# Kernel tuning notes

Measured on AMD Instinct MI355X. Metric: run time of the kernel, lower is better.

## Reference

```python
import jax, jax.numpy as jnp
import numpy as np

# static config matching init_kwargs / setup
T = 0.1      # temperature
MARG = 0.0   # margin m
NEG_IOU = 0.5
K = 1        # pos_topk
WEIGHT = 1.0
P = 2080     # number of True entries in mask2d (triu of 64x64)


def _normalize(x, axis=-1, eps=1e-12):
    n = jnp.sqrt(jnp.sum(x * x, axis=axis, keepdims=True))
    return x / jnp.maximum(n, eps)


def _log_ce(pos_scores, all_scores, neg_mask, t, m):
    # pos_scores: (..., K); all_scores: (..., K or 1, L); neg_mask broadcastable to all_scores
    pos_logit = (pos_scores - m) / t
    pos_exp = jnp.exp(pos_logit)
    neg_exp_sum = jnp.sum(jnp.exp(all_scores / t) * neg_mask.astype(all_scores.dtype), axis=-1)
    loss = -(pos_logit - jnp.log(pos_exp + neg_exp_sum))
    return jnp.mean(loss)


def setup_inputs() -> dict:
    key = jax.random.key(0)
    k1, k2, k3, k4 = jax.random.split(key, 4)
    S, C, N, B, M = 64, 256, 64, 16, 128
    video_feats = jax.random.normal(k1, (S, C, N, N), dtype=jnp.float32)
    sents_feats = jax.random.normal(k2, (S, C), dtype=jnp.float32)
    iou2d = jax.random.uniform(k3, (S, N, N), dtype=jnp.float32)
    iou2ds = jax.random.uniform(k4, (M, N, N), dtype=jnp.float32)
    num_sentences = jnp.full((B,), 4, dtype=jnp.int32)   # sum == S
    num_targets = jnp.full((S,), 2, dtype=jnp.int32)     # sum == M
    mask2d = jnp.triu(jnp.ones((N, N), dtype=bool))      # P = 2080 valid proposals
    return {
        "video_feats": video_feats, "sents_feats": sents_feats,
        "iou2d": iou2d, "iou2ds": iou2ds,
        "num_sentences": num_sentences, "num_targets": num_targets,
        "mask2d": mask2d,
    }


def reference(video_feats, sents_feats, iou2d, iou2ds, num_sentences, num_targets, mask2d):
    S, C, N, _ = video_feats.shape
    B = num_sentences.shape[0]
    M = iou2ds.shape[0]

    # flat proposal indices (static count P)
    mask_idx = jnp.nonzero(mask2d.reshape(-1), size=P)[0]

    # scatter maps
    scatter_b2s = jnp.concatenate([jnp.zeros((1,), jnp.int32),
                                   jnp.cumsum(num_sentences)[:-1].astype(jnp.int32)])  # (B,)
    scatter_m2s = jnp.repeat(jnp.arange(S), num_targets, total_repeat_length=M)        # (M,)
    scatter_s2b = jnp.repeat(jnp.arange(B), num_sentences, total_repeat_length=S)      # (S,)

    # select valid proposals: (S,C,P) -> (S,P,C)
    vf = video_feats.reshape(S, C, N * N)[:, :, mask_idx].transpose(0, 2, 1)
    iou2d_f = iou2d.reshape(S, N * N)[:, mask_idx]    # (S,P)
    iou2ds_f = iou2ds.reshape(M, N * N)[:, mask_idx]  # (M,P)

    vf = _normalize(vf, axis=-1)          # (S,P,C)
    sf = _normalize(sents_feats, axis=-1) # (S,C)

    # top-K proposals per moment
    topk_idxs = jax.lax.top_k(iou2ds_f, K)[1]                         # (M,K)
    allm_vf = vf[scatter_m2s]                                         # (M,P,C)
    topk_vf = jnp.take_along_axis(allm_vf, topk_idxs[:, :, None], 1)  # (M,K,C)

    # inter-video loss
    inter_video_pos = jnp.sum(topk_vf * sf[scatter_m2s][:, None, :], axis=-1)  # (M,K)
    inter_video_all = jnp.einsum('mkc,sc->mks', topk_vf, sf)                   # (M,K,S)
    eye_mask = ~jnp.eye(S, dtype=bool)
    inter_video_neg_mask = eye_mask[scatter_m2s][:, None, :]                   # (M,1,S)
    loss_inter_video = _log_ce(inter_video_pos, inter_video_all, inter_video_neg_mask, T, MARG)

    # inter-query loss
    inter_query_pos = inter_video_pos                                  # (M,K)
    vf_b = vf[scatter_b2s].reshape(B * P, C)                           # one sentence-rep per video
    inter_query_all = jnp.einsum('sc,qc->sq', sf, vf_b)[:, None, :]    # (S,1,B*P)

    # pos_mask: row s has its video block b=scatter_s2b[s] set to (iou2d > neg_iou)
    s2v_pos = iou2d_f > NEG_IOU                                        # (S,P)
    pos_mask = jnp.zeros((S, B, P), dtype=bool)
    pos_mask = pos_mask.at[jnp.arange(S), scatter_s2b].set(s2v_pos)
    pos_mask = pos_mask.reshape(S, B * P)
    inter_query_neg_mask = (~pos_mask)[:, None, :]                     # (S,1,B*P)

    loss_inter_query = _log_ce(inter_query_pos,
                               inter_query_all[scatter_m2s],
                               inter_query_neg_mask[scatter_m2s], T, MARG)

    return (loss_inter_video + loss_inter_query) * WEIGHT
```

## Files before the change

### kernel.cpp

```cpp
#include <hip/hip_runtime.h>
#include <math.h>

#define C 256
#define NN 4096
#define SDIM 64
#define T_INV 10.0f
#define NEG_IOU_TH 0.5f
#define SG 32
#define QTILE 256
#define QTILES (NN / QTILE)

__device__ __forceinline__ float wave_reduce_sum(float v) {
    #pragma unroll
    for (int off = 32; off > 0; off >>= 1) v += __shfl_xor(v, off, 64);
    return v;
}

__global__ void k_prep(const float* __restrict__ sents,
                       const int* __restrict__ num_sentences,
                       const int* __restrict__ num_targets,
                       int B, int S, int M,
                       float* __restrict__ sfT, int* __restrict__ b2s,
                       int* __restrict__ s2b, int* __restrict__ m2s,
                       float* __restrict__ denomq, int* __restrict__ counter) {
    __shared__ float red[4];
    int s = blockIdx.x, tid = threadIdx.x;
    float v = sents[(size_t)s * C + tid];
    float ssq = wave_reduce_sum(v * v);
    int lane = tid & 63, wave = tid >> 6;
    if (lane == 0) red[wave] = ssq;
    __syncthreads();
    float tot = red[0] + red[1] + red[2] + red[3];
    sfT[(size_t)tid * S + s] = v * (1.0f / fmaxf(sqrtf(tot), 1e-12f));

    if (blockIdx.x == 0) {
        if (tid < S) denomq[tid] = 0.f;
        if (tid == 0) {
            *counter = 0;
            int acc = 0;
            for (int b = 0; b < B; ++b) {
                b2s[b] = acc;
                int nsb = num_sentences[b];
                for (int k = 0; k < nsb; ++k) s2b[acc + k] = b;
                acc += nsb;
            }
            int mi = 0;
            for (int si = 0; si < S; ++si) {
                int nt = num_targets[si];
                for (int k = 0; k < nt; ++k) m2s[mi++] = si;
            }
        }
    }
}

__global__ void __launch_bounds__(256)
k_main(const float* __restrict__ vf, const float* __restrict__ iou2d,
       const float* __restrict__ iou2ds, const int* __restrict__ num_sentences,
       const float* __restrict__ sfT, const int* __restrict__ b2s,
       const int* __restrict__ m2s,
       float* __restrict__ pos, float* __restrict__ negiv,
       float* __restrict__ denomq, int* __restrict__ counter,
       float* __restrict__ out, int S, int B, int M, int nq, int ntot) {
    __shared__ float red[4];
    __shared__ int   sidx[4];
    __shared__ float dw[4][SDIM];
    __shared__ int   bestflat;
    __shared__ int   amlast;
    __shared__ float tv[C];
    __shared__ float sc4[256];

    int bid = blockIdx.x, tid = threadIdx.x;
    int lane = tid & 63, wave = tid >> 6;

    if (bid >= M) {
        int qb   = bid - M;
        int tile = qb & (QTILES - 1);
        int rem  = qb >> 4;
        int b    = rem & 15;
        int g    = rem >> 4;
        int sb = b2s[b];
        int ns = num_sentences[b];

        int flat = tile * QTILE + tid;
        const float* vp = vf + (size_t)sb * C * NN + flat;
        const float4* sq = (const float4*)sfT + (size_t)g * 8;

        float acc[SG];
        #pragma unroll
        for (int s = 0; s < SG; ++s) acc[s] = 0.f;
        float ssq = 0.f;

        #pragma unroll 4
        for (int c = 0; c < C; ++c) {
            float v = vp[(size_t)c * NN];
            ssq += v * v;
            const float4* sqc = sq + (size_t)c * (SDIM / 4);
            #pragma unroll
            for (int k = 0; k < SG / 4; ++k) {
                float4 q4 = sqc[k];
                acc[k * 4 + 0] += q4.x * v;
                acc[k * 4 + 1] += q4.y * v;
                acc[k * 4 + 2] += q4.z * v;
                acc[k * 4 + 3] += q4.w * v;
            }
        }

        int r = flat >> 6, cc = flat & 63;
        bool valid = (cc >= r);
        float scale = (1.0f / fmaxf(sqrtf(ssq), 1e-12f)) * T_INV;

        unsigned long long excl = 0ull;
        for (int i = 0; i < ns; ++i)
            if (iou2d[(size_t)(sb + i) * NN + flat] > NEG_IOU_TH)
                excl |= (1ull << (sb + i));
        if (!valid) excl = ~0ull;

        unsigned mask32 = (unsigned)(excl >> (g * 32));
        #pragma unroll
        for (int i = 0; i < SG; ++i)
            acc[i] = ((mask32 >> i) & 1u) ? 0.f : expf(acc[i] * scale);

        #pragma unroll
        for (int off = 16; off >= 1; off >>= 1) {
            int bsel = lane & off;
            #pragma unroll
            for (int i = 0; i < off; ++i) {
                float keep = bsel ? acc[off + i] : acc[i];
                float send = bsel ? acc[i] : acc[off + i];
                acc[i] = keep + __shfl_xor(send, off, 64);
            }
        }
        float tot_s = acc[0] + __shfl_xor(acc[0], 32, 64);
        if (lane < 32) dw[wave][lane] = tot_s;
        __syncthreads();
        if (tid < 32)
            atomicAdd(&denomq[g * 32 + tid],
                      dw[0][tid] + dw[1][tid] + dw[2][tid] + dw[3][tid]);
    } else {
        int m = bid;
        int s_m = m2s[m];

        float bv = -1e30f; int bi = NN;
        #pragma unroll
        for (int j = 0; j < NN / 256; ++j) {
            int flat = tid + j * 256;
            int rr = flat >> 6, cc = flat & 63;
            if (cc >= rr) {
                float val = iou2ds[(size_t)m * NN + flat];
                if (val > bv || (val == bv && flat < bi)) { bv = val; bi = flat; }
            }
        }
        #pragma unroll
        for (int off = 32; off > 0; off >>= 1) {
            float ov = __shfl_xor(bv, off, 64);
            int   oi = __shfl_xor(bi, off, 64);
            if (ov > bv || (ov == bv && oi < bi)) { bv = ov; bi = oi; }
        }
        if (lane == 0) { red[wave] = bv; sidx[wave] = bi; }
        __syncthreads();
        if (tid == 0) {
            float v0 = red[0]; int i0 = sidx[0];
            for (int w = 1; w < 4; ++w)
                if (red[w] > v0 || (red[w] == v0 && sidx[w] < i0)) { v0 = red[w]; i0 = sidx[w]; }
            bestflat = i0;
        }
        __syncthreads();
        int flat = bestflat;

        float v = vf[((size_t)s_m * C + tid) * NN + flat];
        float ssq = wave_reduce_sum(v * v);
        if (lane == 0) red[wave] = ssq;
        __syncthreads();
        float tot = red[0] + red[1] + red[2] + red[3];
        tv[tid] = v * (1.0f / fmaxf(sqrtf(tot), 1e-12f));
        __syncthreads();

        {
            int s = tid & 63, cg = tid >> 6;
            float d = 0.f;
            for (int j = 0; j < 64; ++j) {
                int c2 = cg * 64 + j;
                d += tv[c2] * sfT[(size_t)c2 * S + s];
            }
            sc4[cg * 64 + s] = d;
        }
        __syncthreads();
        if (tid < 64) {
            float d = sc4[tid] + sc4[64 + tid] + sc4[128 + tid] + sc4[192 + tid];
            if (tid == s_m) atomicExch(&pos[m], d);
            float e = (tid == s_m) ? 0.f : expf(d * T_INV);
            e = wave_reduce_sum(e);
            if (tid == 0) atomicExch(&negiv[m], e);
        }
    }

    __syncthreads();
    if (tid == 0) {
        __threadfence();
        int old = atomicAdd(counter, 1);
        amlast = (old == ntot - 1) ? 1 : 0;
    }
    __syncthreads();
    if (!amlast) return;

    __threadfence();
    float val = 0.f;
    for (int m = tid; m < M; m += 256) {
        int s = m2s[m];
        float pl  = atomicAdd(&pos[m], 0.f) * T_INV;
        float niv = atomicAdd(&negiv[m], 0.f);
        float dq  = atomicAdd(&denomq[s], 0.f);
        float pe = expf(pl);
        val += -(pl - logf(pe + niv)) + -(pl - logf(pe + dq));
    }
    val = wave_reduce_sum(val);
    if (lane == 0) dw[0][wave] = val;
    __syncthreads();
    if (tid == 0) out[0] = (dw[0][0] + dw[0][1] + dw[0][2] + dw[0][3]) / (float)M;
}

extern "C" void kernel_launch(void* const* d_in, const int* in_sizes, int n_in,
                              void* d_out, int out_size, void* d_ws, size_t ws_size,
                              hipStream_t stream) {
    const float* video_feats   = (const float*)d_in[0];
    const float* sents_feats   = (const float*)d_in[1];
    const float* iou2d         = (const float*)d_in[2];
    const float* iou2ds        = (const float*)d_in[3];
    const int*   num_sentences = (const int*)d_in[4];
    const int*   num_targets   = (const int*)d_in[5];

    const int S = in_sizes[2] / NN;
    const int B = in_sizes[4];
    const int M = in_sizes[3] / NN;

    float* sfT    = (float*)d_ws;
    float* pos    = sfT + (size_t)C * 64;
    float* negiv  = pos + M;
    float* denomq = negiv + M;
    int*   b2s    = (int*)(denomq + S);
    int*   s2b    = b2s + B;
    int*   m2s    = s2b + S;
    int*   counter = m2s + M;

    const int nq   = QTILES * B * (SDIM / SG);
    const int ntot = M + nq;

    k_prep<<<S, C, 0, stream>>>(sents_feats, num_sentences, num_targets,
                                B, S, M, sfT, b2s, s2b, m2s, denomq, counter);
    k_main<<<ntot, 256, 0, stream>>>(video_feats, iou2d, iou2ds, num_sentences,
                                     sfT, b2s, m2s, pos, negiv, denomq, counter,
                                     (float*)d_out, S, B, M, nq, ntot);
}
```

Baseline: 383.7 us.

## Fuse prep into main kernel, stage sentence tile in LDS, two proposals per thread

```diff
diff --git a/kernel.cpp b/kernel.cpp
--- a/kernel.cpp
+++ b/kernel.cpp
@@ -7,8 +7,10 @@
 #define T_INV 10.0f
 #define NEG_IOU_TH 0.5f
 #define SG 32
-#define QTILE 256
-#define QTILES (NN / QTILE)
+#define FL 2
+#define QT (256 * FL)
+#define QTILES (NN / QT)
+#define PAD 36
 
 __device__ __forceinline__ float wave_reduce_sum(float v) {
     #pragma unroll
@@ -16,58 +18,19 @@
     return v;
 }
 
-__global__ void k_prep(const float* __restrict__ sents,
-                       const int* __restrict__ num_sentences,
-                       const int* __restrict__ num_targets,
-                       int B, int S, int M,
-                       float* __restrict__ sfT, int* __restrict__ b2s,
-                       int* __restrict__ s2b, int* __restrict__ m2s,
-                       float* __restrict__ denomq, int* __restrict__ counter) {
-    __shared__ float red[4];
-    int s = blockIdx.x, tid = threadIdx.x;
-    float v = sents[(size_t)s * C + tid];
-    float ssq = wave_reduce_sum(v * v);
-    int lane = tid & 63, wave = tid >> 6;
-    if (lane == 0) red[wave] = ssq;
-    __syncthreads();
-    float tot = red[0] + red[1] + red[2] + red[3];
-    sfT[(size_t)tid * S + s] = v * (1.0f / fmaxf(sqrtf(tot), 1e-12f));
-
-    if (blockIdx.x == 0) {
-        if (tid < S) denomq[tid] = 0.f;
-        if (tid == 0) {
-            *counter = 0;
-            int acc = 0;
-            for (int b = 0; b < B; ++b) {
-                b2s[b] = acc;
-                int nsb = num_sentences[b];
-                for (int k = 0; k < nsb; ++k) s2b[acc + k] = b;
-                acc += nsb;
-            }
-            int mi = 0;
-            for (int si = 0; si < S; ++si) {
-                int nt = num_targets[si];
-                for (int k = 0; k < nt; ++k) m2s[mi++] = si;
-            }
-        }
-    }
-}
-
 __global__ void __launch_bounds__(256)
-k_main(const float* __restrict__ vf, const float* __restrict__ iou2d,
-       const float* __restrict__ iou2ds, const int* __restrict__ num_sentences,
-       const float* __restrict__ sfT, const int* __restrict__ b2s,
-       const int* __restrict__ m2s,
-       float* __restrict__ pos, float* __restrict__ negiv,
+k_main(const float* __restrict__ vf, const float* __restrict__ sents,
+       const float* __restrict__ iou2d, const float* __restrict__ iou2ds,
+       const int* __restrict__ num_sentences, const int* __restrict__ num_targets,
        float* __restrict__ denomq, int* __restrict__ counter,
-       float* __restrict__ out, int S, int B, int M, int nq, int ntot) {
+       float* __restrict__ pos, float* __restrict__ negiv, int* __restrict__ msent,
+       float* __restrict__ out, int S, int B, int M, int ntot) {
+    __shared__ float smem[C * PAD + SG];
     __shared__ float red[4];
     __shared__ int   sidx[4];
-    __shared__ float dw[4][SDIM];
+    __shared__ float dw[4][SG];
     __shared__ int   bestflat;
     __shared__ int   amlast;
-    __shared__ float tv[C];
-    __shared__ float sc4[256];
 
     int bid = blockIdx.x, tid = threadIdx.x;
     int lane = tid & 63, wave = tid >> 6;
@@ -75,77 +38,122 @@
     if (bid >= M) {
         int qb   = bid - M;
         int tile = qb & (QTILES - 1);
-        int rem  = qb >> 4;
-        int b    = rem & 15;
-        int g    = rem >> 4;
-        int sb = b2s[b];
+        int b    = (qb >> 3) & 15;
+        int g    = qb >> 7;
+
+        int sb = 0;
+        for (int i = 0; i < b; ++i) sb += num_sentences[i];
         int ns = num_sentences[b];
 
-        int flat = tile * QTILE + tid;
-        const float* vp = vf + (size_t)sb * C * NN + flat;
-        const float4* sq = (const float4*)sfT + (size_t)g * 8;
-
-        float acc[SG];
-        #pragma unroll
-        for (int s = 0; s < SG; ++s) acc[s] = 0.f;
-        float ssq = 0.f;
-
-        #pragma unroll 4
+        float* sT = smem;
+        float* sn = smem + C * PAD;
+        if (tid < SG) sn[tid] = 0.f;
+        __syncthreads();
+        {
+            int s  = tid >> 3;
+            int c0 = (tid & 7) * 32;
+            const float* sp = sents + (size_t)(g * SG + s) * C + c0;
+            float ssq = 0.f;
+            #pragma unroll
+            for (int j = 0; j < 32; j += 4) {
+                float4 x = *(const float4*)(sp + j);
+                sT[(c0 + j + 0) * PAD + s] = x.x;
+                sT[(c0 + j + 1) * PAD + s] = x.y;
+                sT[(c0 + j + 2) * PAD + s] = x.z;
+                sT[(c0 + j + 3) * PAD + s] = x.w;
+                ssq += x.x*x.x + x.y*x.y + x.z*x.z + x.w*x.w;
+            }
+            atomicAdd(&sn[s], ssq);
+        }
+        __syncthreads();
+        if (tid < SG) sn[tid] = 1.0f / fmaxf(sqrtf(sn[tid]), 1e-12f);
+        __syncthreads();
+
+        int flat0 = tile * QT + tid * FL;
+        const float2* vp = (const float2*)(vf + (size_t)sb * C * NN + flat0);
+
+        float accA[SG], accB[SG];
+        #pragma unroll
+        for (int i = 0; i < SG; ++i) { accA[i] = 0.f; accB[i] = 0.f; }
+        float ssx = 0.f, ssy = 0.f;
+
+        #pragma unroll 2
         for (int c = 0; c < C; ++c) {
-            float v = vp[(size_t)c * NN];
-            ssq += v * v;
-            const float4* sqc = sq + (size_t)c * (SDIM / 4);
+            float2 v = vp[(size_t)c * (NN / 2)];
+            ssx += v.x * v.x; ssy += v.y * v.y;
+            const float4* sr = (const float4*)&sT[c * PAD];
             #pragma unroll
             for (int k = 0; k < SG / 4; ++k) {
-                float4 q4 = sqc[k];
-                acc[k * 4 + 0] += q4.x * v;
-                acc[k * 4 + 1] += q4.y * v;
-                acc[k * 4 + 2] += q4.z * v;
-                acc[k * 4 + 3] += q4.w * v;
-            }
-        }
-
-        int r = flat >> 6, cc = flat & 63;
-        bool valid = (cc >= r);
-        float scale = (1.0f / fmaxf(sqrtf(ssq), 1e-12f)) * T_INV;
-
-        unsigned long long excl = 0ull;
-        for (int i = 0; i < ns; ++i)
-            if (iou2d[(size_t)(sb + i) * NN + flat] > NEG_IOU_TH)
-                excl |= (1ull << (sb + i));
-        if (!valid) excl = ~0ull;
-
-        unsigned mask32 = (unsigned)(excl >> (g * 32));
-        #pragma unroll
-        for (int i = 0; i < SG; ++i)
-            acc[i] = ((mask32 >> i) & 1u) ? 0.f : expf(acc[i] * scale);
+                float4 q4 = sr[k];
+                accA[k*4+0] += q4.x * v.x;  accB[k*4+0] += q4.x * v.y;
+                accA[k*4+1] += q4.y * v.x;  accB[k*4+1] += q4.y * v.y;
+                accA[k*4+2] += q4.z * v.x;  accB[k*4+2] += q4.z * v.y;
+                accA[k*4+3] += q4.w * v.x;  accB[k*4+3] += q4.w * v.y;
+            }
+        }
+
+        int fA = flat0, fB = flat0 + 1;
+        bool vA = ((fA & 63) >= (fA >> 6));
+        bool vB = ((fB & 63) >= (fB >> 6));
+        float sclA = (1.0f / fmaxf(sqrtf(ssx), 1e-12f)) * T_INV;
+        float sclB = (1.0f / fmaxf(sqrtf(ssy), 1e-12f)) * T_INV;
+
+        unsigned long long bitsA = 0ull, bitsB = 0ull;
+        for (int i = 0; i < ns; ++i) {
+            const float* row = iou2d + (size_t)(sb + i) * NN;
+            if (vA && row[fA] > NEG_IOU_TH) bitsA |= (1ull << (sb + i));
+            if (vB && row[fB] > NEG_IOU_TH) bitsB |= (1ull << (sb + i));
+        }
+        unsigned mA = vA ? (unsigned)(bitsA >> (g * SG)) : 0xffffffffu;
+        unsigned mB = vB ? (unsigned)(bitsB >> (g * SG)) : 0xffffffffu;
+
+        #pragma unroll
+        for (int i = 0; i < SG; ++i) {
+            float inv = sn[i];
+            float e = 0.f;
+            if (!((mA >> i) & 1u)) e += expf(accA[i] * inv * sclA);
+            if (!((mB >> i) & 1u)) e += expf(accB[i] * inv * sclB);
+            accA[i] = e;
+        }
 
         #pragma unroll
         for (int off = 16; off >= 1; off >>= 1) {
             int bsel = lane & off;
             #pragma unroll
             for (int i = 0; i < off; ++i) {
-                float keep = bsel ? acc[off + i] : acc[i];
-                float send = bsel ? acc[i] : acc[off + i];
-                acc[i] = keep + __shfl_xor(send, off, 64);
-            }
-        }
-        float tot_s = acc[0] + __shfl_xor(acc[0], 32, 64);
+                float keep = bsel ? accA[off + i] : accA[i];
+                float send = bsel ? accA[i] : accA[off + i];
+                accA[i] = keep + __shfl_xor(send, off, 64);
+            }
+        }
+        float tot_s = accA[0] + __shfl_xor(accA[0], 32, 64);
         if (lane < 32) dw[wave][lane] = tot_s;
         __syncthreads();
-        if (tid < 32)
-            atomicAdd(&denomq[g * 32 + tid],
+        if (tid < SG)
+            atomicAdd(&denomq[g * SG + tid],
                       dw[0][tid] + dw[1][tid] + dw[2][tid] + dw[3][tid]);
     } else {
         int m = bid;
-        int s_m = m2s[m];
+        int s_m = 0;
+        {
+            int acc2 = 0;
+            for (int s2 = 0; s2 < SDIM; ++s2) {
+                int nt = num_targets[s2];
+                if (m >= acc2 && m < acc2 + nt) s_m = s2;
+                acc2 += nt;
+            }
+        }
+
+        float* tv = smem;
+        float* pd = smem + C;
+        float* ps = smem + C + 256;
 
         float bv = -1e30f; int bi = NN;
         #pragma unroll
         for (int j = 0; j < NN / 256; ++j) {
             int flat = tid + j * 256;
-            int rr = flat >> 6, cc = flat & 63;
-            if (cc >= rr) {
+            int rr = flat >> 6, cc2 = flat & 63;
+            if (cc2 >= rr) {
                 float val = iou2ds[(size_t)m * NN + flat];
                 if (val > bv || (val == bv && flat < bi)) { bv = val; bi = flat; }
             }
@@ -176,21 +184,28 @@
         __syncthreads();
 
         {
-            int s = tid & 63, cg = tid >> 6;
-            float d = 0.f;
-            for (int j = 0; j < 64; ++j) {
-                int c2 = cg * 64 + j;
-                d += tv[c2] * sfT[(size_t)c2 * S + s];
-            }
-            sc4[cg * 64 + s] = d;
-        }
-        __syncthreads();
-        if (tid < 64) {
-            float d = sc4[tid] + sc4[64 + tid] + sc4[128 + tid] + sc4[192 + tid];
-            if (tid == s_m) atomicExch(&pos[m], d);
-            float e = (tid == s_m) ? 0.f : expf(d * T_INV);
+            int s2 = tid >> 2, q = tid & 3;
+            const float4* sp = (const float4*)(sents + (size_t)s2 * C + q * 64);
+            const float4* tp = (const float4*)(tv + q * 64);
+            float d = 0.f, ss = 0.f;
+            #pragma unroll
+            for (int j = 0; j < 16; ++j) {
+                float4 x = sp[j];
+                float4 t = tp[j];
+                d  += x.x*t.x + x.y*t.y + x.z*t.z + x.w*t.w;
+                ss += x.x*x.x + x.y*x.y + x.z*x.z + x.w*x.w;
+            }
+            pd[tid] = d; ps[tid] = ss;
+        }
+        __syncthreads();
+        if (tid < SDIM) {
+            float dt = pd[tid*4+0] + pd[tid*4+1] + pd[tid*4+2] + pd[tid*4+3];
+            float st = ps[tid*4+0] + ps[tid*4+1] + ps[tid*4+2] + ps[tid*4+3];
+            float dd = dt * (1.0f / fmaxf(sqrtf(st), 1e-12f));
+            if (tid == s_m) atomicExch(&pos[m], dd);
+            float e = (tid == s_m) ? 0.f : expf(dd * T_INV);
             e = wave_reduce_sum(e);
-            if (tid == 0) atomicExch(&negiv[m], e);
+            if (tid == 0) { atomicExch(&negiv[m], e); atomicExch(&msent[m], s_m); }
         }
     }
 
@@ -205,11 +220,11 @@
 
     __threadfence();
     float val = 0.f;
-    for (int m = tid; m < M; m += 256) {
-        int s = m2s[m];
-        float pl  = atomicAdd(&pos[m], 0.f) * T_INV;
-        float niv = atomicAdd(&negiv[m], 0.f);
-        float dq  = atomicAdd(&denomq[s], 0.f);
+    for (int m2 = tid; m2 < M; m2 += 256) {
+        int   sm2 = atomicAdd(&msent[m2], 0);
+        float pl  = atomicAdd(&pos[m2], 0.f) * T_INV;
+        float niv = atomicAdd(&negiv[m2], 0.f);
+        float dq  = atomicAdd(&denomq[sm2], 0.f);
         float pe = expf(pl);
         val += -(pl - logf(pe + niv)) + -(pl - logf(pe + dq));
     }
@@ -233,21 +248,19 @@
     const int B = in_sizes[4];
     const int M = in_sizes[3] / NN;
 
-    float* sfT    = (float*)d_ws;
-    float* pos    = sfT + (size_t)C * 64;
-    float* negiv  = pos + M;
-    float* denomq = negiv + M;
-    int*   b2s    = (int*)(denomq + S);
-    int*   s2b    = b2s + B;
-    int*   m2s    = s2b + S;
-    int*   counter = m2s + M;
+    float* denomq  = (float*)d_ws;
+    int*   counter = (int*)(denomq + SDIM);
+    float* pos     = (float*)(counter + 1);
+    float* negiv   = pos + M;
+    int*   msent   = (int*)(negiv + M);
+
+    hipMemsetAsync(d_ws, 0, (SDIM + 1) * sizeof(float), stream);
 
     const int nq   = QTILES * B * (SDIM / SG);
     const int ntot = M + nq;
 
-    k_prep<<<S, C, 0, stream>>>(sents_feats, num_sentences, num_targets,
-                                B, S, M, sfT, b2s, s2b, m2s, denomq, counter);
-    k_main<<<ntot, 256, 0, stream>>>(video_feats, iou2d, iou2ds, num_sentences,
-                                     sfT, b2s, m2s, pos, negiv, denomq, counter,
-                                     (float*)d_out, S, B, M, nq, ntot);
+    k_main<<<ntot, 256, 0, stream>>>(video_feats, sents_feats, iou2d, iou2ds,
+                                     num_sentences, num_targets,
+                                     denomq, counter, pos, negiv, msent,
+                                     (float*)d_out, S, B, M, ntot);
 }
```

Result: slower. 463.2 us (+20.7%).
